# Kernel tuning notes

Hardware: AMD Instinct MI355X
Metric: run time of the kernel (lower is better)

Reference implementation:

```python
import jax, jax.numpy as jnp
import numpy as np

H = 6  # num_heads
D = 384  # embedding_dim


def _rot(seg, coord):
    # seg: [BN, H, T, L], coord: [BN, T]; rotate interleaved even/odd pairs
    L = seg.shape[-1]
    pairs = max(L // 2, 1)
    inv_freq = 1.0 / (10000.0 ** (jnp.arange(pairs, dtype=seg.dtype) / pairs))
    ang = coord[..., None] * inv_freq          # [BN, T, pairs]
    cos = jnp.cos(ang)[:, None]                # [BN, 1, T, pairs]
    sin = jnp.sin(ang)[:, None]
    even, odd = seg[..., 0::2], seg[..., 1::2]
    re = even * cos - odd * sin
    ro = even * sin + odd * cos
    return jnp.stack((re, ro), axis=-1).reshape(seg.shape)


def _apply_rope3(t, pos, chunk):
    # t: [BN, H, T, Hd], pos: [BN, T, 3]; three axis chunks, tail untouched
    parts, s = [], 0
    for i in range(3):
        parts.append(_rot(t[..., s:s + chunk], pos[..., i]))
        s += chunk
    parts.append(t[..., s:])
    return jnp.concatenate(parts, axis=-1)


def setup_inputs() -> dict:
    key = jax.random.key(0)
    ks = jax.random.split(key, 10)
    B, N, T = 8, 64, 128
    scale = 1.0 / np.sqrt(D)
    return {
        "padded_batches": jax.random.normal(ks[0], (B, N, T, D), jnp.float32),
        "sum_token": jax.random.normal(ks[1], (B, N, 1, D), jnp.float32),
        "positions_3d": jax.random.uniform(ks[2], (B, N, T, 3), jnp.float32),
        "Wq": jax.random.normal(ks[3], (D, D), jnp.float32) * scale,
        "bq": jax.random.normal(ks[4], (D,), jnp.float32) * scale,
        "Wk": jax.random.normal(ks[5], (D, D), jnp.float32) * scale,
        "bk": jax.random.normal(ks[6], (D,), jnp.float32) * scale,
        "Wv": jax.random.normal(ks[7], (D, D), jnp.float32) * scale,
        "bv": jax.random.normal(ks[8], (D,), jnp.float32) * scale,
        "masks": jax.random.randint(ks[9], (B, N, T), 0, 2, jnp.int32),
    }


def reference(padded_batches, sum_token, positions_3d, Wq, bq, Wk, bk, Wv, bv, masks):
    B, N, T, Dm = padded_batches.shape
    Hd = Dm // H
    chunk = Hd // 6 * 2

    # masked mean-pool summary token (summary_mode='avg')
    w = masks[..., None].astype(padded_batches.dtype)          # [B,N,T,1]
    denom = jnp.clip(w.sum(axis=-2, keepdims=True), 1e-6, None)
    summary = (padded_batches * w).sum(axis=-2, keepdims=True) / denom  # [B,N,1,D]

    q = (padded_batches @ Wq + bq).reshape(B * N, T, H, Hd).transpose(0, 2, 1, 3)  # [BN,H,T,Hd]
    k = (summary @ Wk + bk).reshape(B * N, 1, H, Hd).transpose(0, 2, 1, 3)         # [BN,H,1,Hd]
    v = (summary @ Wv + bv).reshape(B * N, 1, H, Hd).transpose(0, 2, 1, 3)

    # 3-axis RoPE on q (token positions) and k (pooled positions)
    pos_summary = (positions_3d * w).sum(axis=-2, keepdims=True) / denom  # [B,N,1,3]
    pos_q = positions_3d.reshape(B * N, T, 3)
    pos_k = pos_summary.reshape(B * N, 1, 3)
    q = _apply_rope3(q, pos_q, chunk)
    k = _apply_rope3(k, pos_k, chunk)

    # SDPA with T queries vs 1 key
    scores = jnp.einsum('bhtd,bhkd->bhtk', q, k) / np.float32(np.sqrt(Hd))  # [BN,H,T,1]
    mask_add = jnp.where(masks.reshape(B * N, 1, T, 1) == 0,
                         jnp.finfo(jnp.float32).min, 0.0)
    attn_w = jax.nn.softmax(scores + mask_add, axis=-1)
    attn = jnp.einsum('bhtk,bhkd->bhtd', attn_w, v)  # [BN,H,T,Hd]

    out = attn.transpose(0, 2, 1, 3).reshape(B, N, T, Dm) + padded_batches
    return out
```

## Files before the change

kernel.cpp:

```cpp
#include <hip/hip_runtime.h>


#define DM 384
#define TT 128
#define C4 96
#define BN_TOT 512
#define NR  8
#define RPT 16

__global__ __launch_bounds__(768) void fused_mean_matvec_add(
    const float* __restrict__ padded,
    const int*   __restrict__ masks,
    const float* __restrict__ Wv,
    const float* __restrict__ bv,
    float*       __restrict__ out)
{
    const int bn = blockIdx.x;
    const int t  = threadIdx.x;
    const int c  = t % C4;
    const int r  = t / C4;

    __shared__ float  w_sh[TT];
    __shared__ float4 part_sh[NR][C4];
    __shared__ float  summ[DM];
    __shared__ float4 v_sh[C4];

    const float4* __restrict__ p4 =
        (const float4*)padded + (size_t)bn * TT * C4;

    float4 x[RPT];
    #pragma unroll
    for (int i = 0; i < RPT; ++i) {
        x[i] = p4[(r + i * NR) * C4 + c];
    }

    if (t < TT) w_sh[t] = (float)masks[bn * TT + t];
    __syncthreads();

    float4 acc = make_float4(0.f, 0.f, 0.f, 0.f);
    #pragma unroll
    for (int i = 0; i < RPT; ++i) {
        const float w = w_sh[r + i * NR];
        acc.x += x[i].x * w; acc.y += x[i].y * w;
        acc.z += x[i].z * w; acc.w += x[i].w * w;
    }
    part_sh[r][c] = acc;
    __syncthreads();

    if (t < C4) {
        float dsum = 0.f;
        #pragma unroll
        for (int i = 0; i < TT; ++i) dsum += w_sh[i];
        const float inv = 1.0f / fmaxf(dsum, 1e-6f);

        float4 s = part_sh[0][t];
        #pragma unroll
        for (int g = 1; g < NR; ++g) {
            const float4 p = part_sh[g][t];
            s.x += p.x; s.y += p.y; s.z += p.z; s.w += p.w;
        }
        s.x *= inv; s.y *= inv; s.z *= inv; s.w *= inv;
        ((float4*)summ)[t] = s;
    }
    __syncthreads();

    float4 a = make_float4(0.f, 0.f, 0.f, 0.f);
    const float4* __restrict__ wv4 = (const float4*)Wv;
    const int e0 = r * (DM / NR);
    #pragma unroll 8
    for (int i = 0; i < DM / NR; ++i) {
        const int   e = e0 + i;
        const float s = summ[e];
        const float4 w = wv4[(size_t)e * C4 + c];
        a.x += s * w.x; a.y += s * w.y; a.z += s * w.z; a.w += s * w.w;
    }
    part_sh[r][c] = a;
    __syncthreads();

    if (t < C4) {
        float4 v = ((const float4*)bv)[t];
        #pragma unroll
        for (int g = 0; g < NR; ++g) {
            const float4 p = part_sh[g][t];
            v.x += p.x; v.y += p.y; v.z += p.z; v.w += p.w;
        }
        v_sh[t] = v;
    }
    __syncthreads();

    const float4 v = v_sh[c];
    float4* __restrict__ o4 = (float4*)out + (size_t)bn * TT * C4;
    #pragma unroll
    for (int i = 0; i < RPT; ++i) {
        float4 y = x[i];
        y.x += v.x; y.y += v.y; y.z += v.z; y.w += v.w;
        o4[(r + i * NR) * C4 + c] = y;
    }
}

extern "C" void kernel_launch(void* const* d_in, const int* in_sizes, int n_in,
                              void* d_out, int out_size, void* d_ws, size_t ws_size,
                              hipStream_t stream) {
    const float* padded = (const float*)d_in[0];
    const float* Wv     = (const float*)d_in[7];
    const float* bv     = (const float*)d_in[8];
    const int*   masks  = (const int*)d_in[9];
    float* out = (float*)d_out;

    fused_mean_matvec_add<<<BN_TOT, 768, 0, stream>>>(padded, masks, Wv, bv, out);
}
```

Before: 211.8 us.

## Restructure block to 384 threads with wave-shuffle reductions and nontemporal stores

Block size drops from 768 to 384 threads. Each wave now owns a 16-column slice, so both the masked-mean and the matvec reductions are done with cross-lane shuffles instead of shared-memory partials, which removes most __syncthreads. The input tile is no longer kept in registers. It is re-read from global memory for the final residual add, and outputs use nontemporal stores. This trades extra global reads, which may hit cache, for less synchronisation and lower register pressure.

```diff
diff --git a/kernel.cpp b/kernel.cpp
--- a/kernel.cpp
+++ b/kernel.cpp
@@ -5,96 +5,93 @@
 #define TT 128
 #define C4 96
 #define BN_TOT 512
-#define NR  8
-#define RPT 16
 
-__global__ __launch_bounds__(768) void fused_mean_matvec_add(
+typedef float f32x4 __attribute__((ext_vector_type(4)));
+
+__device__ __forceinline__ void nt_store4(float4* p, const float4 v) {
+    __builtin_nontemporal_store(*(const f32x4*)&v, (f32x4*)p);
+}
+
+__global__ __launch_bounds__(384) void fused_wave(
     const float* __restrict__ padded,
     const int*   __restrict__ masks,
     const float* __restrict__ Wv,
     const float* __restrict__ bv,
     float*       __restrict__ out)
 {
-    const int bn = blockIdx.x;
-    const int t  = threadIdx.x;
-    const int c  = t % C4;
-    const int r  = t / C4;
+    const int bn   = blockIdx.x;
+    const int t    = threadIdx.x;
+    const int lane = t & 63;
+    const int wid  = t >> 6;
+    const int colg = lane & 15;
+    const int rg   = lane >> 4;
+    const int c4   = wid * 16 + colg;
 
-    __shared__ float  w_sh[TT];
-    __shared__ float4 part_sh[NR][C4];
-    __shared__ float  summ[DM];
-    __shared__ float4 v_sh[C4];
+    __shared__ float summ_sh[DM];
 
-    const float4* __restrict__ p4 =
-        (const float4*)padded + (size_t)bn * TT * C4;
+    const float4* __restrict__ p4 = (const float4*)padded + (size_t)bn * TT * C4;
+    const int*    __restrict__ mk = masks + bn * TT;
 
-    float4 x[RPT];
+    float4 a0 = make_float4(0.f, 0.f, 0.f, 0.f);
+    float4 a1 = make_float4(0.f, 0.f, 0.f, 0.f);
+    float  ws0 = 0.f, ws1 = 0.f;
     #pragma unroll
-    for (int i = 0; i < RPT; ++i) {
-        x[i] = p4[(r + i * NR) * C4 + c];
+    for (int j = 0; j < 16; ++j) {
+        const int rA = rg + 8 * j;
+        const int rB = rA + 4;
+        const float wA = (float)mk[rA];
+        const float wB = (float)mk[rB];
+        const float4 xA = p4[rA * C4 + c4];
+        const float4 xB = p4[rB * C4 + c4];
+        a0.x += xA.x * wA; a0.y += xA.y * wA; a0.z += xA.z * wA; a0.w += xA.w * wA;
+        a1.x += xB.x * wB; a1.y += xB.y * wB; a1.z += xB.z * wB; a1.w += xB.w * wB;
+        ws0 += wA; ws1 += wB;
     }
+    a0.x += a1.x; a0.y += a1.y; a0.z += a1.z; a0.w += a1.w;
+    ws0 += ws1;
 
-    if (t < TT) w_sh[t] = (float)masks[bn * TT + t];
-    __syncthreads();
-
-    float4 acc = make_float4(0.f, 0.f, 0.f, 0.f);
     #pragma unroll
-    for (int i = 0; i < RPT; ++i) {
-        const float w = w_sh[r + i * NR];
-        acc.x += x[i].x * w; acc.y += x[i].y * w;
-        acc.z += x[i].z * w; acc.w += x[i].w * w;
+    for (int m = 16; m < 64; m <<= 1) {
+        a0.x += __shfl_xor(a0.x, m, 64);
+        a0.y += __shfl_xor(a0.y, m, 64);
+        a0.z += __shfl_xor(a0.z, m, 64);
+        a0.w += __shfl_xor(a0.w, m, 64);
+        ws0  += __shfl_xor(ws0,  m, 64);
     }
-    part_sh[r][c] = acc;
-    __syncthreads();
-
-    if (t < C4) {
-        float dsum = 0.f;
-        #pragma unroll
-        for (int i = 0; i < TT; ++i) dsum += w_sh[i];
-        const float inv = 1.0f / fmaxf(dsum, 1e-6f);
-
-        float4 s = part_sh[0][t];
-        #pragma unroll
-        for (int g = 1; g < NR; ++g) {
-            const float4 p = part_sh[g][t];
-            s.x += p.x; s.y += p.y; s.z += p.z; s.w += p.w;
-        }
-        s.x *= inv; s.y *= inv; s.z *= inv; s.w *= inv;
-        ((float4*)summ)[t] = s;
+    const float inv = 1.0f / fmaxf(ws0, 1e-6f);
+    if (rg == 0) {
+        float4 s;
+        s.x = a0.x * inv; s.y = a0.y * inv; s.z = a0.z * inv; s.w = a0.w * inv;
+        ((float4*)summ_sh)[c4] = s;
     }
     __syncthreads();
 
-    float4 a = make_float4(0.f, 0.f, 0.f, 0.f);
+    float4 v = make_float4(0.f, 0.f, 0.f, 0.f);
     const float4* __restrict__ wv4 = (const float4*)Wv;
-    const int e0 = r * (DM / NR);
     #pragma unroll 8
-    for (int i = 0; i < DM / NR; ++i) {
-        const int   e = e0 + i;
-        const float s = summ[e];
-        const float4 w = wv4[(size_t)e * C4 + c];
-        a.x += s * w.x; a.y += s * w.y; a.z += s * w.z; a.w += s * w.w;
+    for (int j = 0; j < C4; ++j) {
+        const int   e = rg + 4 * j;
+        const float s = summ_sh[e];
+        const float4 w = wv4[(size_t)e * C4 + c4];
+        v.x += s * w.x; v.y += s * w.y; v.z += s * w.z; v.w += s * w.w;
     }
-    part_sh[r][c] = a;
-    __syncthreads();
+    #pragma unroll
+    for (int m = 16; m < 64; m <<= 1) {
+        v.x += __shfl_xor(v.x, m, 64);
+        v.y += __shfl_xor(v.y, m, 64);
+        v.z += __shfl_xor(v.z, m, 64);
+        v.w += __shfl_xor(v.w, m, 64);
+    }
+    const float4 b = ((const float4*)bv)[c4];
+    v.x += b.x; v.y += b.y; v.z += b.z; v.w += b.w;
 
-    if (t < C4) {
-        float4 v = ((const float4*)bv)[t];
-        #pragma unroll
-        for (int g = 0; g < NR; ++g) {
-            const float4 p = part_sh[g][t];
-            v.x += p.x; v.y += p.y; v.z += p.z; v.w += p.w;
-        }
-        v_sh[t] = v;
-    }
-    __syncthreads();
-
-    const float4 v = v_sh[c];
     float4* __restrict__ o4 = (float4*)out + (size_t)bn * TT * C4;
     #pragma unroll
-    for (int i = 0; i < RPT; ++i) {
-        float4 y = x[i];
-        y.x += v.x; y.y += v.y; y.z += v.z; y.w += v.w;
-        o4[(r + i * NR) * C4 + c] = y;
+    for (int j = 0; j < 32; ++j) {
+        const int r = rg + 4 * j;
+        float4 x = p4[r * C4 + c4];
+        x.x += v.x; x.y += v.y; x.z += v.z; x.w += v.w;
+        nt_store4(&o4[r * C4 + c4], x);
     }
 }
 
@@ -107,5 +104,5 @@
     const int*   masks  = (const int*)d_in[9];
     float* out = (float*)d_out;
 
-    fused_mean_matvec_add<<<BN_TOT, 768, 0, stream>>>(padded, masks, Wv, bv, out);
+    fused_wave<<<BN_TOT, 384, 0, stream>>>(padded, masks, Wv, bv, out);
 }
```

Result: no change. 215.0 us (+1.5%).

## Split fused kernel into partial-sum and matvec-add kernels with more blocks

Applied to the files above, without the earlier changes.

Replaces the single 512-block fused kernel with two kernels. The first computes masked partial row sums over quarter-token slices into a workspace using 2048 blocks. The second reduces the partials, runs the Wv matvec split across two column halves, and re-reads padded to add v, using nontemporal stores. The aim is higher occupancy and more parallelism in the memory-bound reduction, at the cost of reading the input twice plus an extra launch and workspace round trip.

```diff
diff --git a/kernel.cpp b/kernel.cpp
--- a/kernel.cpp
+++ b/kernel.cpp
@@ -5,96 +5,129 @@
 #define TT 128
 #define C4 96
 #define BN_TOT 512
-#define NR  8
-#define RPT 16
 
-__global__ __launch_bounds__(768) void fused_mean_matvec_add(
+typedef float f32x4 __attribute__((ext_vector_type(4)));
+
+__device__ __forceinline__ void nt_store4(float4* p, const float4 v) {
+    __builtin_nontemporal_store(*(const f32x4*)&v, (f32x4*)p);
+}
+
+__global__ __launch_bounds__(384) void k_partial(
     const float* __restrict__ padded,
     const int*   __restrict__ masks,
+    float*       __restrict__ ws_part,
+    float*       __restrict__ ws_cnt)
+{
+    const int b  = blockIdx.x;
+    const int bn = b >> 2;
+    const int q  = b & 3;
+    const int t  = threadIdx.x;
+    const int c  = t % C4;
+    const int rr = t / C4;
+
+    __shared__ float  w_sh[32];
+    __shared__ float4 part[4][C4];
+
+    if (t < 32) w_sh[t] = (float)masks[bn * TT + q * 32 + t];
+    __syncthreads();
+
+    const float4* __restrict__ p4 =
+        (const float4*)padded + (size_t)bn * TT * C4 + (size_t)q * 32 * C4;
+
+    float4 acc = make_float4(0.f, 0.f, 0.f, 0.f);
+    #pragma unroll
+    for (int j = 0; j < 8; ++j) {
+        const int   r = rr + 4 * j;
+        const float w = w_sh[r];
+        const float4 x = p4[r * C4 + c];
+        acc.x += x.x * w; acc.y += x.y * w; acc.z += x.z * w; acc.w += x.w * w;
+    }
+    part[rr][c] = acc;
+    __syncthreads();
+
+    if (t < C4) {
+        const float4 a0 = part[0][t], a1 = part[1][t];
+        const float4 a2 = part[2][t], a3 = part[3][t];
+        float4 s;
+        s.x = (a0.x + a1.x) + (a2.x + a3.x);
+        s.y = (a0.y + a1.y) + (a2.y + a3.y);
+        s.z = (a0.z + a1.z) + (a2.z + a3.z);
+        s.w = (a0.w + a1.w) + (a2.w + a3.w);
+        ((float4*)(ws_part + ((size_t)bn * 4 + q) * DM))[t] = s;
+    } else if (t == C4) {
+        float s0 = 0.f, s1 = 0.f, s2 = 0.f, s3 = 0.f;
+        #pragma unroll
+        for (int i = 0; i < 8; ++i) {
+            s0 += w_sh[i];      s1 += w_sh[8 + i];
+            s2 += w_sh[16 + i]; s3 += w_sh[24 + i];
+        }
+        ws_cnt[bn * 4 + q] = (s0 + s1) + (s2 + s3);
+    }
+}
+
+__global__ __launch_bounds__(384) void k_final_add(
+    const float* __restrict__ padded,
+    const float* __restrict__ ws_part,
+    const float* __restrict__ ws_cnt,
     const float* __restrict__ Wv,
     const float* __restrict__ bv,
     float*       __restrict__ out)
 {
-    const int bn = blockIdx.x;
+    const int b  = blockIdx.x;
+    const int bn = b >> 1;
+    const int h  = b & 1;
     const int t  = threadIdx.x;
-    const int c  = t % C4;
-    const int r  = t / C4;
+    const int c4 = t % 48;
+    const int g8 = t / 48;
 
-    __shared__ float  w_sh[TT];
-    __shared__ float4 part_sh[NR][C4];
     __shared__ float  summ[DM];
-    __shared__ float4 v_sh[C4];
+    __shared__ float4 mpart[8][48];
+    __shared__ float4 v_sh[48];
 
-    const float4* __restrict__ p4 =
-        (const float4*)padded + (size_t)bn * TT * C4;
-
-    float4 x[RPT];
-    #pragma unroll
-    for (int i = 0; i < RPT; ++i) {
-        x[i] = p4[(r + i * NR) * C4 + c];
-    }
-
-    if (t < TT) w_sh[t] = (float)masks[bn * TT + t];
-    __syncthreads();
-
-    float4 acc = make_float4(0.f, 0.f, 0.f, 0.f);
-    #pragma unroll
-    for (int i = 0; i < RPT; ++i) {
-        const float w = w_sh[r + i * NR];
-        acc.x += x[i].x * w; acc.y += x[i].y * w;
-        acc.z += x[i].z * w; acc.w += x[i].w * w;
-    }
-    part_sh[r][c] = acc;
-    __syncthreads();
-
-    if (t < C4) {
-        float dsum = 0.f;
-        #pragma unroll
-        for (int i = 0; i < TT; ++i) dsum += w_sh[i];
-        const float inv = 1.0f / fmaxf(dsum, 1e-6f);
-
-        float4 s = part_sh[0][t];
-        #pragma unroll
-        for (int g = 1; g < NR; ++g) {
-            const float4 p = part_sh[g][t];
-            s.x += p.x; s.y += p.y; s.z += p.z; s.w += p.w;
-        }
-        s.x *= inv; s.y *= inv; s.z *= inv; s.w *= inv;
-        ((float4*)summ)[t] = s;
+    {
+        const float* __restrict__ pp = ws_part + (size_t)bn * 4 * DM;
+        const float  s = (pp[t] + pp[DM + t]) + (pp[2 * DM + t] + pp[3 * DM + t]);
+        const float* __restrict__ cc = ws_cnt + bn * 4;
+        const float  cnt = (cc[0] + cc[1]) + (cc[2] + cc[3]);
+        summ[t] = s * (1.0f / fmaxf(cnt, 1e-6f));
     }
     __syncthreads();
 
-    float4 a = make_float4(0.f, 0.f, 0.f, 0.f);
-    const float4* __restrict__ wv4 = (const float4*)Wv;
-    const int e0 = r * (DM / NR);
-    #pragma unroll 8
-    for (int i = 0; i < DM / NR; ++i) {
-        const int   e = e0 + i;
-        const float s = summ[e];
-        const float4 w = wv4[(size_t)e * C4 + c];
-        a.x += s * w.x; a.y += s * w.y; a.z += s * w.z; a.w += s * w.w;
+    {
+        float4 a = make_float4(0.f, 0.f, 0.f, 0.f);
+        const float4* __restrict__ wv4 = (const float4*)Wv;
+        #pragma unroll 6
+        for (int j = 0; j < 48; ++j) {
+            const int   e = g8 * 48 + j;
+            const float s = summ[e];
+            const float4 w = wv4[(size_t)e * C4 + h * 48 + c4];
+            a.x += s * w.x; a.y += s * w.y; a.z += s * w.z; a.w += s * w.w;
+        }
+        mpart[g8][c4] = a;
     }
-    part_sh[r][c] = a;
     __syncthreads();
 
-    if (t < C4) {
-        float4 v = ((const float4*)bv)[t];
+    if (t < 48) {
+        float4 v = ((const float4*)bv)[h * 48 + t];
         #pragma unroll
-        for (int g = 0; g < NR; ++g) {
-            const float4 p = part_sh[g][t];
+        for (int g = 0; g < 8; ++g) {
+            const float4 p = mpart[g][t];
             v.x += p.x; v.y += p.y; v.z += p.z; v.w += p.w;
         }
         v_sh[t] = v;
     }
     __syncthreads();
 
-    const float4 v = v_sh[c];
-    float4* __restrict__ o4 = (float4*)out + (size_t)bn * TT * C4;
+    const float4* __restrict__ p4 = (const float4*)padded + (size_t)bn * TT * C4;
+    float4*       __restrict__ o4 = (float4*)out + (size_t)bn * TT * C4;
+    const float4 v = v_sh[c4];
     #pragma unroll
-    for (int i = 0; i < RPT; ++i) {
-        float4 y = x[i];
-        y.x += v.x; y.y += v.y; y.z += v.z; y.w += v.w;
-        o4[(r + i * NR) * C4 + c] = y;
+    for (int j = 0; j < 16; ++j) {
+        const int    r   = g8 + 8 * j;
+        const size_t idx = (size_t)r * C4 + h * 48 + c4;
+        float4 x = p4[idx];
+        x.x += v.x; x.y += v.y; x.z += v.z; x.w += v.w;
+        nt_store4(&o4[idx], x);
     }
 }
 
@@ -107,5 +140,10 @@
     const int*   masks  = (const int*)d_in[9];
     float* out = (float*)d_out;
 
-    fused_mean_matvec_add<<<BN_TOT, 768, 0, stream>>>(padded, masks, Wv, bv, out);
+    float* ws_part = (float*)d_ws;
+    float* ws_cnt  = ws_part + (size_t)BN_TOT * 4 * DM;
+
+    k_partial<<<BN_TOT * 4, 384, 0, stream>>>(padded, masks, ws_part, ws_cnt);
+    k_final_add<<<BN_TOT * 2, 384, 0, stream>>>(padded, ws_part, ws_cnt,
+                                                Wv, bv, out);
 }
```

Measured after the change: 215.6 us. Within noise of the previous version (+1.8%).
